# Kernel tuning notes

Hardware: AMD Instinct MI355X
Metric: run time of the kernel (lower is better)

Reference implementation:

```python
import jax, jax.numpy as jnp
import numpy as np

EPS = 1e-5  # torch GroupNorm default


def setup_inputs() -> dict:
    key = jax.random.key(0)
    ks = jax.random.split(key, 7)
    B, H, W, C = 8, 64, 64, 64
    x = jax.random.normal(ks[0], (B, H, W, C), dtype=jnp.float32)
    temb = jax.random.normal(ks[1], (B, 256), dtype=jnp.float32)
    scale = 0.02
    Wq = jax.random.normal(ks[2], (C, C), dtype=jnp.float32) * scale
    Wk = jax.random.normal(ks[3], (C, C), dtype=jnp.float32) * scale
    Wv = jax.random.normal(ks[4], (C, C), dtype=jnp.float32) * scale
    Wo = jax.random.normal(ks[5], (C, C), dtype=jnp.float32) * scale
    z = jnp.zeros((C,), dtype=jnp.float32)
    return {"x": x, "temb": temb, "Wq": Wq, "bq": z, "Wk": Wk, "bk": z,
            "Wv": Wv, "bv": z, "Wo": Wo, "bo": z}


def reference(x, temb, Wq, bq, Wk, bk, Wv, bv, Wo, bo):
    # x: [B, H, W, C] channels-last. temb is accepted but unused (as in source).
    B, H, W, C = x.shape
    S = H * W
    # normalize(): freshly-built GroupNorm(num_groups=1) with identity affine
    # -> standardize over all non-batch dims.
    mu = jnp.mean(x, axis=(1, 2, 3), keepdims=True)
    var = jnp.var(x, axis=(1, 2, 3), keepdims=True)
    h = (x - mu) * jax.lax.rsqrt(var + EPS)
    hf = h.reshape(B, S, C)
    q = hf @ Wq.T + bq  # [B, S, C]
    k = hf @ Wk.T + bk
    v = hf @ Wv.T + bv
    # full (S x S) score matrix, scaled by C^-0.5, naive softmax
    w = jnp.einsum('bsc,btc->bst', q, k) * (C ** -0.5)
    w = jax.nn.softmax(w, axis=-1)
    o = jnp.einsum('bst,btc->bsc', w, v)  # [B, S, C]
    o = o @ Wo.T + bo
    return x + o.reshape(B, H, W, C)
```

## Files before the change

kernel.cpp:

```cpp
#include <hip/hip_runtime.h>
#include <hip/hip_bf16.h>
#include <math.h>

#define B_ 8
#define S_ 4096
#define C_ 64
#define EPSV 1e-5f

using floatx4 = __attribute__((ext_vector_type(4))) float;
using bf16x8  = __attribute__((ext_vector_type(8))) short;
using bf16x4  = __attribute__((ext_vector_type(4))) short;

typedef __attribute__((address_space(3))) unsigned int       as3_u32;
typedef __attribute__((address_space(1))) const unsigned int as1_u32;

__device__ __forceinline__ short f2bf(float f) {
    unsigned u = __builtin_bit_cast(unsigned, f);
    u = u + 0x7fffu + ((u >> 16) & 1u);
    return (short)(u >> 16);
}

__device__ __forceinline__ float bf2f(short s) {
    return __builtin_bit_cast(float, ((unsigned)(unsigned short)s) << 16);
}

__device__ __forceinline__ unsigned cvt_pk_bf16(float lo, float hi) {
    unsigned r;
    asm volatile("v_cvt_pk_bf16_f32 %0, %1, %2" : "=v"(r) : "v"(lo), "v"(hi));
    return r;
}

__device__ __forceinline__ floatx4 mfma_16x16x16_bf16(bf16x4 a, bf16x4 b, floatx4 c) {
#if __has_builtin(__builtin_amdgcn_mfma_f32_16x16x16bf16_1k)
    return __builtin_amdgcn_mfma_f32_16x16x16bf16_1k(a, b, c, 0, 0, 0);
#else
    asm("v_mfma_f32_16x16x16_bf16 %0, %1, %2, %0" : "+v"(c) : "v"(a), "v"(b));
    return c;
#endif
}

__device__ __forceinline__ bf16x8 ld_w_frag(const float* __restrict__ W, int n, int kk, int g, int c) {
    const float* p = W + (16 * n + c) * C_ + 32 * kk + 8 * g;
    bf16x8 r;
#pragma unroll
    for (int j = 0; j < 8; ++j) r[j] = f2bf(p[j]);
    return r;
}

__global__ __launch_bounds__(256) void stats1_kernel(const float* __restrict__ x,
                                                     float* __restrict__ partial) {
    int b = blockIdx.x >> 5, chunk = blockIdx.x & 31;
    const float4* xb = (const float4*)x + (size_t)b * 65536 + chunk * 2048;
    float s = 0.f, ss = 0.f;
#pragma unroll
    for (int i = 0; i < 8; ++i) {
        float4 v = xb[threadIdx.x + i * 256];
        s  += v.x + v.y + v.z + v.w;
        ss += v.x * v.x + v.y * v.y + v.z * v.z + v.w * v.w;
    }
    for (int off = 32; off > 0; off >>= 1) {
        s  += __shfl_down(s, off);
        ss += __shfl_down(ss, off);
    }
    __shared__ float sm[4], ssm[4];
    int wid = threadIdx.x >> 6, lane = threadIdx.x & 63;
    if (lane == 0) { sm[wid] = s; ssm[wid] = ss; }
    __syncthreads();
    if (threadIdx.x == 0) {
        partial[blockIdx.x * 2]     = sm[0] + sm[1] + sm[2] + sm[3];
        partial[blockIdx.x * 2 + 1] = ssm[0] + ssm[1] + ssm[2] + ssm[3];
    }
}

__global__ __launch_bounds__(512) void stats2_kernel(const float* __restrict__ partial,
                                                     float* __restrict__ stats) {
    int w = threadIdx.x >> 6, lane = threadIdx.x & 63;
    float s = 0.f, ss = 0.f;
    if (lane < 32) {
        s  = partial[(w * 32 + lane) * 2];
        ss = partial[(w * 32 + lane) * 2 + 1];
    }
    for (int off = 16; off > 0; off >>= 1) {
        s  += __shfl_down(s, off);
        ss += __shfl_down(ss, off);
    }
    if (lane == 0) {
        const float invN = 1.0f / (float)(S_ * C_);
        float mu  = s * invN;
        float var = ss * invN - mu * mu;
        stats[w * 2]     = mu;
        stats[w * 2 + 1] = rsqrtf(var + EPSV);
    }
}

__global__ __launch_bounds__(256) void proj_kernel(
    const float* __restrict__ x,
    const float* __restrict__ Wq, const float* __restrict__ bq,
    const float* __restrict__ Wk, const float* __restrict__ bk,
    const float* __restrict__ Wv, const float* __restrict__ bv,
    const float* __restrict__ stats,
    short* __restrict__ qo, char* __restrict__ kws, char* __restrict__ vws) {
    __shared__ char hbuf[64 * 128];

    int b  = blockIdx.x >> 6;
    int t_ = blockIdx.x & 63;
    int s0 = t_ * 64;
    float mu = stats[b * 2], rs = stats[b * 2 + 1];
    const float* xt = x + ((size_t)b * S_ + s0) * C_;
    int t = threadIdx.x;

#pragma unroll
    for (int i = 0; i < 4; ++i) {
        int fi  = t + 256 * i;
        int row = fi >> 4;
        int c4  = fi & 15;
        float4 v = *(const float4*)(xt + row * C_ + c4 * 4);
        unsigned lo = (unsigned)(unsigned short)f2bf((v.x - mu) * rs) |
                      ((unsigned)(unsigned short)f2bf((v.y - mu) * rs) << 16);
        unsigned hi = (unsigned)(unsigned short)f2bf((v.z - mu) * rs) |
                      ((unsigned)(unsigned short)f2bf((v.w - mu) * rs) << 16);
        int off = row * 128 + c4 * 8;
        off ^= (row & 7) << 4;
        *(uint2*)(hbuf + off) = make_uint2(lo, hi);
    }
    __syncthreads();

    int lane = t & 63, w = t >> 6;
    int g = lane >> 4, c = lane & 15;

    auto ld_h = [&](int row, int kcol) -> bf16x8 {
        int off = row * 128 + kcol * 2;
        off ^= (row & 7) << 4;
        return *(const bf16x8*)(hbuf + off);
    };

    bf16x8 ha[2];
    ha[0] = ld_h(16 * w + c, 8 * g);
    ha[1] = ld_h(16 * w + c, 32 + 8 * g);

    const float QSC = 0.125f * 1.44269504088896340736f;

#pragma unroll
    for (int n = 0; n < 4; ++n) {
        floatx4 aq = {0.f, 0.f, 0.f, 0.f}, ak = {0.f, 0.f, 0.f, 0.f};
#pragma unroll
        for (int kk = 0; kk < 2; ++kk) {
            bf16x8 wq = ld_w_frag(Wq, n, kk, g, c);
            bf16x8 wk = ld_w_frag(Wk, n, kk, g, c);
            aq = __builtin_amdgcn_mfma_f32_16x16x32_bf16(ha[kk], wq, aq, 0, 0, 0);
            ak = __builtin_amdgcn_mfma_f32_16x16x32_bf16(ha[kk], wk, ak, 0, 0, 0);
        }
        float bqv = bq[16 * n + c], bkv = bk[16 * n + c];
#pragma unroll
        for (int r = 0; r < 4; ++r) {
            int rr = 16 * w + 4 * g + r;
            qo[((size_t)b * S_ + s0 + rr) * C_ + 16 * n + c] = f2bf((aq[r] + bqv) * QSC);
            int r32 = rr & 31;
            size_t tb = ((size_t)b * 128 + 2 * t_ + (rr >> 5)) * 4096;
            int koff = (r32 * 128 + (16 * n + c) * 2) ^ ((r32 & 7) << 4);
            *(short*)(kws + tb + koff) = f2bf(ak[r] + bkv);
        }
    }

    bf16x8 wv[2];
    wv[0] = ld_w_frag(Wv, w, 0, g, c);
    wv[1] = ld_w_frag(Wv, w, 1, g, c);
    float bvr[4];
#pragma unroll
    for (int r = 0; r < 4; ++r) bvr[r] = bv[16 * w + 4 * g + r];

#pragma unroll
    for (int n = 0; n < 4; ++n) {
        floatx4 av = {0.f, 0.f, 0.f, 0.f};
#pragma unroll
        for (int kk = 0; kk < 2; ++kk) {
            bf16x8 hb = ld_h(16 * n + c, 32 * kk + 8 * g);
            av = __builtin_amdgcn_mfma_f32_16x16x32_bf16(wv[kk], hb, av, 0, 0, 0);
        }
        int u   = 16 * n + c;
        int u32 = u & 31;
        size_t tb = ((size_t)b * 128 + 2 * t_ + (u >> 5)) * 4096;
#pragma unroll
        for (int r = 0; r < 4; ++r) {
            int rr = 16 * w + 4 * g + r;
            int voff = (rr * 64 + u32 * 2) ^ ((rr & 7) << 3);
            *(short*)(vws + tb + voff) = f2bf(av[r] + bvr[r]);
        }
    }
}

__global__ __launch_bounds__(256, 4) void flash_kernel(
    const short* __restrict__ qm, const char* __restrict__ kws, const char* __restrict__ vws,
    short* __restrict__ Opart, float2* __restrict__ mlpart) {
    __shared__ char lds[16384];

    int bid = blockIdx.x;
    int logical = (bid & 7) * 128 + (bid >> 3);
    int b = logical >> 7;
    int rest = logical & 127;
    int q0 = (rest >> 2) * 128;
    int quarter = rest & 3;
    int t = threadIdx.x;
    int lane = t & 63, w = t >> 6;
    int g = lane >> 4, c = lane & 15;
    int qw = q0 + 32 * w;

    const char* kbase = kws + (size_t)b * 128 * 4096;
    const char* vbase = vws + (size_t)b * 128 * 4096;
    const short* qp = qm + (size_t)b * S_ * C_;

    bf16x8 bqf[2][2];
#pragma unroll
    for (int qi = 0; qi < 2; ++qi) {
        bqf[qi][0] = *(const bf16x8*)(qp + (qw + 16 * qi + c) * C_ + 8 * g);
        bqf[qi][1] = *(const bf16x8*)(qp + (qw + 16 * qi + c) * C_ + 32 + 8 * g);
    }

    floatx4 oacc[2][4];
#pragma unroll
    for (int qi = 0; qi < 2; ++qi)
#pragma unroll
        for (int mi = 0; mi < 4; ++mi) oacc[qi][mi] = (floatx4){0.f, 0.f, 0.f, 0.f};
    float m[2] = {-__builtin_inff(), -__builtin_inff()}, l[2] = {0.f, 0.f};

    const int xmask  = (c & 7) << 4;
    const int vxmask = (c & 7) << 3;

    auto STAGE = [&](int bi, int tt) {
        const char* gk = kbase + (size_t)tt * 4096 + t * 16;
        const char* gv = vbase + (size_t)tt * 4096 + t * 16;
        char* lk = lds +        bi * 4096 + t * 16;
        char* lv = lds + 8192 + bi * 4096 + t * 16;
        __builtin_amdgcn_global_load_lds((as1_u32*)gk, (as3_u32*)lk, 16, 0, 0);
        __builtin_amdgcn_global_load_lds((as1_u32*)gv, (as3_u32*)lv, 16, 0, 0);
    };

    auto ld_k = [&](const char* buf, int s, int colb) -> bf16x8 {
        return *(const bf16x8*)(buf + s * 2048 + c * 128 + (colb ^ xmask));
    };
    auto ld_v = [&](const char* buf, int mi, int s) -> bf16x4 {
        return *(const bf16x4*)(buf + mi * 1024 + c * 64 + ((32 * s + 8 * g) ^ vxmask));
    };

    auto COMPUTE = [&](int bi) {
        const char* kbuf = lds +        bi * 4096;
        const char* vbuf = lds + 8192 + bi * 4096;
        bf16x8 ak[2][2];
#pragma unroll
        for (int s = 0; s < 2; ++s)
#pragma unroll
            for (int kk = 0; kk < 2; ++kk)
                ak[s][kk] = ld_k(kbuf, s, 64 * kk + 16 * g);
        floatx4 st[2][2];
        __builtin_amdgcn_s_setprio(1);
#pragma unroll
        for (int qi = 0; qi < 2; ++qi)
#pragma unroll
            for (int s = 0; s < 2; ++s) {
                st[qi][s] = (floatx4){0.f, 0.f, 0.f, 0.f};
                st[qi][s] = __builtin_amdgcn_mfma_f32_16x16x32_bf16(ak[s][0], bqf[qi][0], st[qi][s], 0, 0, 0);
                st[qi][s] = __builtin_amdgcn_mfma_f32_16x16x32_bf16(ak[s][1], bqf[qi][1], st[qi][s], 0, 0, 0);
            }
        __builtin_amdgcn_s_setprio(0);
        bf16x4 av[2][4];
#pragma unroll
        for (int s = 0; s < 2; ++s)
#pragma unroll
            for (int mi = 0; mi < 4; ++mi)
                av[s][mi] = ld_v(vbuf, mi, s);
        float mt[2], need = -1e30f;
#pragma unroll
        for (int qi = 0; qi < 2; ++qi) {
            float v = fmaxf(fmaxf(st[qi][0][0], st[qi][0][1]), fmaxf(st[qi][0][2], st[qi][0][3]));
            v = fmaxf(v, fmaxf(fmaxf(st[qi][1][0], st[qi][1][1]), fmaxf(st[qi][1][2], st[qi][1][3])));
            v = fmaxf(v, __shfl_xor(v, 16));
            v = fmaxf(v, __shfl_xor(v, 32));
            mt[qi] = v;
            need = fmaxf(need, v - m[qi]);
        }
        if (!__all(need <= 8.0f)) {
#pragma unroll
            for (int qi = 0; qi < 2; ++qi) {
                float mn = fmaxf(m[qi], mt[qi]);
                float a  = __builtin_amdgcn_exp2f(m[qi] - mn);
                m[qi] = mn;
                l[qi] *= a;
#pragma unroll
                for (int mi = 0; mi < 4; ++mi) oacc[qi][mi] *= a;
            }
        }
        bf16x4 pb[2][2];
#pragma unroll
        for (int qi = 0; qi < 2; ++qi) {
            float psum = 0.f;
#pragma unroll
            for (int s = 0; s < 2; ++s) {
                float e0 = __builtin_amdgcn_exp2f(st[qi][s][0] - m[qi]);
                float e1 = __builtin_amdgcn_exp2f(st[qi][s][1] - m[qi]);
                float e2 = __builtin_amdgcn_exp2f(st[qi][s][2] - m[qi]);
                float e3 = __builtin_amdgcn_exp2f(st[qi][s][3] - m[qi]);
                psum += (e0 + e1) + (e2 + e3);
                uint2 u = make_uint2(cvt_pk_bf16(e0, e1), cvt_pk_bf16(e2, e3));
                pb[qi][s] = __builtin_bit_cast(bf16x4, u);
            }
            l[qi] += psum;
        }
        __builtin_amdgcn_s_setprio(1);
#pragma unroll
        for (int qi = 0; qi < 2; ++qi)
#pragma unroll
            for (int s = 0; s < 2; ++s)
#pragma unroll
                for (int mi = 0; mi < 4; ++mi)
                    oacc[qi][mi] = mfma_16x16x16_bf16(av[s][mi], pb[qi][s], oacc[qi][mi]);
        __builtin_amdgcn_s_setprio(0);
    };

    const int base = quarter * 32;
    STAGE(0, base);
    __syncthreads();
    for (int r = 0; r < 32; r += 2) {
        STAGE(1, base + r + 1);
        COMPUTE(0);
        __syncthreads();
        if (r + 2 < 32) STAGE(0, base + r + 2);
        COMPUTE(1);
        __syncthreads();
    }

#pragma unroll
    for (int qi = 0; qi < 2; ++qi) {
        l[qi] += __shfl_xor(l[qi], 16);
        l[qi] += __shfl_xor(l[qi], 32);
    }

    size_t prow = (size_t)(quarter * 8 + b) * S_ + q0;
    if (lane < 16) {
#pragma unroll
        for (int qi = 0; qi < 2; ++qi)
            mlpart[prow + 32 * w + 16 * qi + lane] = make_float2(m[qi], l[qi]);
    }

#pragma unroll
    for (int qi = 0; qi < 2; ++qi) {
        short* op = Opart + (prow + 32 * w + 16 * qi + c) * C_;
#pragma unroll
        for (int mi = 0; mi < 4; ++mi) {
            uint2 u = make_uint2(cvt_pk_bf16(oacc[qi][mi][0], oacc[qi][mi][1]),
                                 cvt_pk_bf16(oacc[qi][mi][2], oacc[qi][mi][3]));
            *(uint2*)(op + 16 * mi + 4 * g) = u;
        }
    }
}

__global__ __launch_bounds__(256) void combine_kernel(
    const short* __restrict__ Opart, const float2* __restrict__ mlpart,
    const float* __restrict__ Wo, const float* __restrict__ bo,
    const float* __restrict__ x, float* __restrict__ out) {
    __shared__ char obuf[8192];

    int bid = blockIdx.x;
    int logical = (bid & 7) * 64 + (bid >> 3);
    int b = logical >> 6;
    int q0 = (logical & 63) * 64;
    int t = threadIdx.x;
    int lane = t & 63, w = t >> 6;
    int g = lane >> 4, c = lane & 15;

    const short*  P[4];
    const float2* ml[4];
#pragma unroll
    for (int h = 0; h < 4; ++h) {
        P[h]  = Opart  + ((size_t)(h * 8 + b) * S_ + q0) * C_;
        ml[h] = mlpart + (size_t)(h * 8 + b) * S_ + q0;
    }

#pragma unroll
    for (int i = 0; i < 16; ++i) {
        int idx = t + 256 * i;
        int q = idx >> 6, ch = idx & 63;
        float2 a0 = ml[0][q], a1 = ml[1][q], a2 = ml[2][q], a3 = ml[3][q];
        float M = fmaxf(fmaxf(a0.x, a1.x), fmaxf(a2.x, a3.x));
        float s0 = __builtin_amdgcn_exp2f(a0.x - M);
        float s1 = __builtin_amdgcn_exp2f(a1.x - M);
        float s2 = __builtin_amdgcn_exp2f(a2.x - M);
        float s3 = __builtin_amdgcn_exp2f(a3.x - M);
        float L  = a0.y * s0 + a1.y * s1 + a2.y * s2 + a3.y * s3;
        float o  = (bf2f(P[0][q * 64 + ch]) * s0 + bf2f(P[1][q * 64 + ch]) * s1 +
                    bf2f(P[2][q * 64 + ch]) * s2 + bf2f(P[3][q * 64 + ch]) * s3) / L;
        int off = (q * 128 + ch * 2) ^ ((q & 7) << 4);
        *(short*)(obuf + off) = f2bf(o);
    }
    __syncthreads();

    bf16x8 ao[2];
    {
        int row = 16 * w + c;
        int off0 = (row * 128 + (8 * g) * 2)      ^ ((row & 7) << 4);
        int off1 = (row * 128 + (32 + 8 * g) * 2) ^ ((row & 7) << 4);
        ao[0] = *(const bf16x8*)(obuf + off0);
        ao[1] = *(const bf16x8*)(obuf + off1);
    }
#pragma unroll
    for (int n = 0; n < 4; ++n) {
        floatx4 a = {0.f, 0.f, 0.f, 0.f};
#pragma unroll
        for (int kk = 0; kk < 2; ++kk) {
            bf16x8 bw = ld_w_frag(Wo, n, kk, g, c);
            a = __builtin_amdgcn_mfma_f32_16x16x32_bf16(ao[kk], bw, a, 0, 0, 0);
        }
        float bov = bo[16 * n + c];
#pragma unroll
        for (int r = 0; r < 4; ++r) {
            int srow = q0 + 16 * w + 4 * g + r;
            size_t idx = ((size_t)b * S_ + srow) * C_ + 16 * n + c;
            out[idx] = x[idx] + bov + a[r];
        }
    }
}

extern "C" void kernel_launch(void* const* d_in, const int* in_sizes, int n_in,
                              void* d_out, int out_size, void* d_ws, size_t ws_size,
                              hipStream_t stream) {
    const float* x  = (const float*)d_in[0];
    const float* Wq = (const float*)d_in[2];
    const float* bq = (const float*)d_in[3];
    const float* Wk = (const float*)d_in[4];
    const float* bk = (const float*)d_in[5];
    const float* Wv = (const float*)d_in[6];
    const float* bv = (const float*)d_in[7];
    const float* Wo = (const float*)d_in[8];
    const float* bo = (const float*)d_in[9];
    float* out = (float*)d_out;

    char* ws = (char*)d_ws;
    float*  partial = (float*)ws;
    float*  stats   = (float*)(ws + 2048);
    short*  q   = (short*)(ws + 4096);
    char*   kt  = (char*)(q + (size_t)B_ * S_ * C_);
    char*   vt  = kt + (size_t)B_ * 128 * 4096;
    short*  op  = (short*)(vt + (size_t)B_ * 128 * 4096);
    float2* mlp = (float2*)((char*)op + (size_t)4 * B_ * S_ * C_ * 2);

    stats1_kernel<<<256, 256, 0, stream>>>(x, partial);
    stats2_kernel<<<1, 512, 0, stream>>>(partial, stats);
    proj_kernel<<<B_ * (S_ / 64), 256, 0, stream>>>(x, Wq, bq, Wk, bk, Wv, bv, stats, q, kt, vt);
    flash_kernel<<<B_ * (S_ / 128) * 4, 256, 0, stream>>>(q, kt, vt, op, mlp);
    combine_kernel<<<B_ * (S_ / 64), 256, 0, stream>>>(op, mlp, Wo, bo, x, out);
}
```

Before: 88.32 us.

## Triple-buffer flash K/V staging and coalesce projection K/V stores via LDS

The flash kernel's K/V staging moves from two buffers to three. Loads are issued two tiles ahead, with explicit vmcnt waits and a single barrier per tile instead of a full __syncthreads drain. Separately, the projection kernel writes its swizzled K and V tiles into shared memory first and then copies them to global with coalesced 16-byte stores, replacing the scattered 2-byte global writes. This costs extra LDS (24KB in flash, 24KB in proj) and relies on hand-tuned waitcnt counts being correct.

```diff
diff --git a/kernel.cpp b/kernel.cpp
--- a/kernel.cpp
+++ b/kernel.cpp
@@ -100,7 +100,9 @@
     const float* __restrict__ Wv, const float* __restrict__ bv,
     const float* __restrict__ stats,
     short* __restrict__ qo, char* __restrict__ kws, char* __restrict__ vws) {
-    __shared__ char hbuf[64 * 128];
+    __shared__ char hbuf[8192];
+    __shared__ char kimg[8192];
+    __shared__ char vimg[8192];
 
     int b  = blockIdx.x >> 6;
     int t_ = blockIdx.x & 63;
@@ -156,9 +158,8 @@
             int rr = 16 * w + 4 * g + r;
             qo[((size_t)b * S_ + s0 + rr) * C_ + 16 * n + c] = f2bf((aq[r] + bqv) * QSC);
             int r32 = rr & 31;
-            size_t tb = ((size_t)b * 128 + 2 * t_ + (rr >> 5)) * 4096;
             int koff = (r32 * 128 + (16 * n + c) * 2) ^ ((r32 & 7) << 4);
-            *(short*)(kws + tb + koff) = f2bf(ak[r] + bkv);
+            *(short*)(kimg + (rr >> 5) * 4096 + koff) = f2bf(ak[r] + bkv);
         }
     }
 
@@ -179,20 +180,27 @@
         }
         int u   = 16 * n + c;
         int u32 = u & 31;
-        size_t tb = ((size_t)b * 128 + 2 * t_ + (u >> 5)) * 4096;
 #pragma unroll
         for (int r = 0; r < 4; ++r) {
             int rr = 16 * w + 4 * g + r;
             int voff = (rr * 64 + u32 * 2) ^ ((rr & 7) << 3);
-            *(short*)(vws + tb + voff) = f2bf(av[r] + bvr[r]);
-        }
+            *(short*)(vimg + (u >> 5) * 4096 + voff) = f2bf(av[r] + bvr[r]);
+        }
+    }
+    __syncthreads();
+
+    size_t gb = ((size_t)b * 128 + 2 * t_) * 4096;
+#pragma unroll
+    for (int i = 0; i < 2; ++i) {
+        *(uint4*)(kws + gb + i * 4096 + t * 16) = *(const uint4*)(kimg + i * 4096 + t * 16);
+        *(uint4*)(vws + gb + i * 4096 + t * 16) = *(const uint4*)(vimg + i * 4096 + t * 16);
     }
 }
 
 __global__ __launch_bounds__(256, 4) void flash_kernel(
     const short* __restrict__ qm, const char* __restrict__ kws, const char* __restrict__ vws,
     short* __restrict__ Opart, float2* __restrict__ mlpart) {
-    __shared__ char lds[16384];
+    __shared__ char lds[24576];
 
     int bid = blockIdx.x;
     int logical = (bid & 7) * 128 + (bid >> 3);
@@ -229,8 +237,8 @@
     auto STAGE = [&](int bi, int tt) {
         const char* gk = kbase + (size_t)tt * 4096 + t * 16;
         const char* gv = vbase + (size_t)tt * 4096 + t * 16;
-        char* lk = lds +        bi * 4096 + t * 16;
-        char* lv = lds + 8192 + bi * 4096 + t * 16;
+        char* lk = lds +         bi * 4096 + t * 16;
+        char* lv = lds + 12288 + bi * 4096 + t * 16;
         __builtin_amdgcn_global_load_lds((as1_u32*)gk, (as3_u32*)lk, 16, 0, 0);
         __builtin_amdgcn_global_load_lds((as1_u32*)gv, (as3_u32*)lv, 16, 0, 0);
     };
@@ -243,8 +251,8 @@
     };
 
     auto COMPUTE = [&](int bi) {
-        const char* kbuf = lds +        bi * 4096;
-        const char* vbuf = lds + 8192 + bi * 4096;
+        const char* kbuf = lds +         bi * 4096;
+        const char* vbuf = lds + 12288 + bi * 4096;
         bf16x8 ak[2][2];
 #pragma unroll
         for (int s = 0; s < 2; ++s)
@@ -318,14 +326,20 @@
 
     const int base = quarter * 32;
     STAGE(0, base);
-    __syncthreads();
-    for (int r = 0; r < 32; r += 2) {
-        STAGE(1, base + r + 1);
-        COMPUTE(0);
-        __syncthreads();
-        if (r + 2 < 32) STAGE(0, base + r + 2);
-        COMPUTE(1);
-        __syncthreads();
+    STAGE(1, base + 1);
+    asm volatile("s_waitcnt vmcnt(2)" ::: "memory");
+    __builtin_amdgcn_s_barrier();
+    __builtin_amdgcn_sched_barrier(0);
+
+    for (int r = 0; r < 32; ++r) {
+        if (r < 30) STAGE((r + 2) % 3, base + r + 2);
+        COMPUTE(r % 3);
+        if (r < 31) {
+            if (r < 30) asm volatile("s_waitcnt vmcnt(2)" ::: "memory");
+            else        asm volatile("s_waitcnt vmcnt(0)" ::: "memory");
+            __builtin_amdgcn_s_barrier();
+            __builtin_amdgcn_sched_barrier(0);
+        }
     }
 
 #pragma unroll
```

Result: no change. 88.63 us (+0.4%).
